# Optimization experiments

Hardware: AMD Instinct MI355X
Metric: run time of the kernel (lower is better)

The kernel has to match this reference:

```python
import jax, jax.numpy as jnp
import numpy as np

H, W = 200, 200           # BEV spatial shape (single level)
NBQ, NH, NL, NP = 2, 8, 1, 4
D = 256
HD = D // NH


def setup_inputs() -> dict:
    key = jax.random.key(0)
    ks = jax.random.split(key, 12)
    bs, nq = 1, H * W
    query = jax.random.normal(ks[0], (bs, nq, D), jnp.float32)
    value = jax.random.normal(ks[1], (bs, NBQ * nq, D), jnp.float32)
    reference_points = jax.random.uniform(ks[2], (bs, nq, NL, 2), dtype=jnp.float32)
    spatial_shapes = jnp.array([[H, W]], dtype=jnp.int32)
    sc = 1.0 / np.sqrt(D)
    W_v = jax.random.normal(ks[3], (D, D), jnp.float32) * sc
    b_v = jax.random.normal(ks[4], (D,), jnp.float32) * 0.01
    W_so = jax.random.normal(ks[5], (2 * D, NBQ * NH * NL * NP * 2), jnp.float32) * 0.02
    b_so = jax.random.normal(ks[6], (NBQ * NH * NL * NP * 2,), jnp.float32) * 0.5
    W_aw = jax.random.normal(ks[7], (2 * D, NBQ * NH * NL * NP), jnp.float32) * 0.02
    b_aw = jax.random.normal(ks[8], (NBQ * NH * NL * NP,), jnp.float32) * 0.01
    W_o = jax.random.normal(ks[9], (D, D), jnp.float32) * sc
    b_o = jax.random.normal(ks[10], (D,), jnp.float32) * 0.01
    return {"query": query, "value": value, "reference_points": reference_points,
            "spatial_shapes": spatial_shapes,
            "W_v": W_v, "b_v": b_v, "W_so": W_so, "b_so": b_so,
            "W_aw": W_aw, "b_aw": b_aw, "W_o": W_o, "b_o": b_o}


def _ms_deform_attn(value, locs, attn):
    # value: (B, K, NH, HD); locs: (B, nq, NH, NL, NP, 2) in [0,1]; attn: (B, nq, NH, NL, NP)
    B, K, h, d = value.shape
    nq = locs.shape[1]
    out = jnp.zeros((B, nq, h, d), value.dtype)
    start = 0
    for l, (Hl, Wl) in enumerate([(H, W)]):
        v = value[:, start:start + Hl * Wl].transpose(0, 2, 1, 3).reshape(B * h, Hl * Wl, d)
        start += Hl * Wl
        g = locs[:, :, :, l]                      # (B, nq, h, NP, 2)
        # grid_sample(align_corners=False, padding='zeros') pixel coords
        x = g[..., 0] * Wl - 0.5
        y = g[..., 1] * Hl - 0.5
        x0 = jnp.floor(x); y0 = jnp.floor(y)
        lx = x - x0; ly = y - y0
        x0 = x0.astype(jnp.int32); y0 = y0.astype(jnp.int32)
        acc = jnp.zeros((B * h, nq * NP, d), value.dtype)
        for dy, wy in ((0, 1.0 - ly), (1, ly)):
            for dx, wx in ((0, 1.0 - lx), (1, lx)):
                xi = x0 + dx; yi = y0 + dy
                valid = ((xi >= 0) & (xi < Wl) & (yi >= 0) & (yi < Hl)).astype(value.dtype)
                idx = jnp.clip(yi, 0, Hl - 1) * Wl + jnp.clip(xi, 0, Wl - 1)  # (B,nq,h,NP)
                idxf = idx.transpose(0, 2, 1, 3).reshape(B * h, nq * NP)
                samp = jnp.take_along_axis(v, idxf[:, :, None], axis=1)       # (B*h, nq*NP, d)
                wgt = (wx * wy * valid).transpose(0, 2, 1, 3).reshape(B * h, nq * NP, 1)
                acc = acc + samp * wgt
        acc = acc.reshape(B, h, nq, NP, d)
        out = out + jnp.einsum('bhqpd,bqhp->bqhd', acc, attn[:, :, :, l])
    return out.reshape(B, nq, h * d)


def reference(query, value, reference_points, spatial_shapes,
              W_v, b_v, W_so, b_so, W_aw, b_aw, W_o, b_o):
    bs, nq, _ = query.shape
    identity = query
    val4 = value.reshape(bs, NBQ, nq, D)
    # query enhanced with most recent bev-queue features
    qe = jnp.concatenate([val4[:, 0], query], axis=-1)           # (bs, nq, 2D)
    vproj = (value @ W_v + b_v).reshape(bs * NBQ, nq, NH, HD)
    off = (qe @ W_so + b_so).reshape(bs, nq, NH, NBQ, NL, NP, 2)
    aw = (qe @ W_aw + b_aw).reshape(bs, nq, NH, NBQ, NL * NP)
    aw = jax.nn.softmax(aw, axis=-1).reshape(bs, nq, NH, NBQ, NL, NP)
    aw = aw.transpose(0, 3, 1, 2, 4, 5).reshape(bs * NBQ, nq, NH, NL, NP)
    # offset normalizer: [W, H] per level
    norm = jnp.stack([spatial_shapes[:, 1], spatial_shapes[:, 0]], -1).astype(query.dtype)  # (NL,2)
    locs = (reference_points[:, :, None, None, :, None, :]
            + off / norm[None, None, None, None, :, None, :])     # (bs,nq,NH,NBQ,NL,NP,2)
    locs = locs.transpose(0, 3, 1, 2, 4, 5, 6).reshape(bs * NBQ, nq, NH, NL, NP, 2)
    out = _ms_deform_attn(vproj, locs, aw)                        # (bs*NBQ, nq, D)
    out = out.reshape(bs, NBQ, nq, D).mean(axis=1)
    return out @ W_o + b_o + identity
```

## Files before the change

### kernel.cpp

```cpp
#include <hip/hip_runtime.h>
#include <math.h>

#define HW_   40000
#define NQ_   40000
#define IMGW  200
#define IMGH  200

typedef __bf16 bf16;
typedef __attribute__((ext_vector_type(4))) __bf16 bf16x4;
typedef __attribute__((ext_vector_type(8))) __bf16 bf16x8;
typedef __attribute__((ext_vector_type(4))) float f32x4;

__device__ __forceinline__ void gload_lds16(const void* g, void* l) {
  __builtin_amdgcn_global_load_lds(
      (const __attribute__((address_space(1))) void*)g,
      (__attribute__((address_space(3))) void*)l, 16, 0, 0);
}

__global__ __launch_bounds__(256) void prep_kernel(
    const float* __restrict__ Wv, const float* __restrict__ Wso,
    const float* __restrict__ Waw, const float* __restrict__ Wo,
    bf16* __restrict__ BtV, bf16* __restrict__ BtOA, bf16* __restrict__ BtO)
{
  int idx = blockIdx.x * 256 + threadIdx.x;
  if (idx < 65536) {
    int k = idx >> 8, n = idx & 255;
    BtV[(size_t)n * 256 + k] = (bf16)Wv[idx];
  } else if (idx < 131072) {
    int j = idx - 65536;
    int k = j >> 7, n = j & 127;
    BtOA[(size_t)n * 512 + k] = (bf16)Wso[j];
  } else if (idx < 163840) {
    int j = idx - 131072;
    int k = j >> 6, n = j & 63;
    BtOA[(size_t)(128 + n) * 512 + k] = (bf16)Waw[j];
  } else if (idx < 229376) {
    int j = idx - 163840;
    int k = j >> 8, n = j & 255;
    BtO[(size_t)n * 256 + k] = (bf16)Wo[j];
  }
}

template<int KT, int MODE, int BN, int ASRC>
__global__ __launch_bounds__(256) void mfma_gemm_kernel(
    const void* __restrict__ A0, const void* __restrict__ A1,
    const bf16* __restrict__ Bt,
    const float* __restrict__ bias0, const float* __restrict__ bias1,
    const float* __restrict__ resid,
    void* __restrict__ outp, void* __restrict__ outp2, int M)
{
  constexpr int NT16 = BN / 32;
  constexpr int NCH  = BN * 4;
  constexpr int BCHN = (NCH + 255) / 256;
  constexpr int NIT  = KT / 32;
  __shared__ bf16 As[2][64 * 32];
  __shared__ bf16 Bs[2][BN * 32];
  const int t    = threadIdx.x;
  const int m0   = blockIdx.x * 64;
  const int n0   = blockIdx.y * BN;
  const int w    = t >> 6;
  const int lane = t & 63;
  const int quad = lane >> 4;
  const int l16  = lane & 15;
  const int wm   = (w & 1) * 32;
  const int wn   = (w >> 1) * (BN / 2);

  f32x4 acc[2][NT16] = {};

  int gmA;
  {
    int gm = m0 + (t >> 2);
    gmA = (gm >= M) ? (M - 1) : gm;
  }
  const int arow = t >> 2;
  const int akey = (arow >> 1) & 3;

  float4 apf[2];
  bf16x8 ah0, ah1;

  auto issueB = [&](int it) {
    const int kt  = it * 32;
    const int buf = it & 1;
#pragma unroll
    for (int i = 0; i < BCHN; ++i) {
      int c = i * 256 + t;
      if (NCH % 256 != 0 && c >= NCH) break;
      int row = c >> 2;
      int j   = (c & 3) ^ ((row >> 1) & 3);
      gload_lds16(&Bt[(size_t)(n0 + row) * KT + kt + j * 8], &Bs[buf][c * 8]);
    }
  };

  auto loadA_reg = [&](int it) {
    const int kt = it * 32;
    if (ASRC == 1) {
      const float* Ap; int col;
      if (KT == 512) { Ap = (kt < 256) ? (const float*)A0 : (const float*)A1; col = kt & 255; }
      else           { Ap = (const float*)A0; col = kt; }
      const float4* s4 = (const float4*)&Ap[(size_t)gmA * 256 + col + (t & 3) * 8];
      apf[0] = s4[0];
      apf[1] = s4[1];
    } else {
      ah0 = *(const bf16x8*)&((const bf16*)A0)[(size_t)gmA * 256 + kt + (t & 3) * 8];
      ah1 = *(const bf16x8*)&((const bf16*)A1)[(size_t)gmA * 256 + kt + (t & 3) * 8];
    }
  };

  auto writeA = [&](int it) {
    const int buf = it & 1;
    int j = (t & 3) ^ akey;
    bf16x8 o;
    if (ASRC == 1) {
      o = bf16x8{(bf16)apf[0].x, (bf16)apf[0].y, (bf16)apf[0].z, (bf16)apf[0].w,
                 (bf16)apf[1].x, (bf16)apf[1].y, (bf16)apf[1].z, (bf16)apf[1].w};
    } else {
#pragma unroll
      for (int e = 0; e < 8; ++e)
        o[e] = (bf16)(0.5f * ((float)ah0[e] + (float)ah1[e]));
    }
    *(bf16x8*)&As[buf][arow * 32 + j * 8] = o;
  };

  loadA_reg(0); issueB(0); writeA(0);

#pragma unroll
  for (int it = 0; it < NIT; ++it) {
    __syncthreads();
    if (it + 1 < NIT) {
      issueB(it + 1);
      loadA_reg(it + 1);
    }
    const bf16* as = As[it & 1];
    const bf16* bs = Bs[it & 1];
    bf16x8 af[2], bfr[NT16];
#pragma unroll
    for (int x = 0; x < 2; ++x) {
      int row = wm + x * 16 + l16;
      af[x] = *(const bf16x8*)&as[row * 32 + (quad ^ ((row >> 1) & 3)) * 8];
    }
#pragma unroll
    for (int x = 0; x < NT16; ++x) {
      int row = wn + x * 16 + l16;
      bfr[x] = *(const bf16x8*)&bs[row * 32 + (quad ^ ((row >> 1) & 3)) * 8];
    }
#pragma unroll
    for (int mt = 0; mt < 2; ++mt)
#pragma unroll
      for (int nt = 0; nt < NT16; ++nt)
        acc[mt][nt] = __builtin_amdgcn_mfma_f32_16x16x32_bf16(
            af[mt], bfr[nt], acc[mt][nt], 0, 0, 0);
    if (it + 1 < NIT) writeA(it + 1);
  }

#pragma unroll
  for (int mt = 0; mt < 2; ++mt) {
#pragma unroll
    for (int r = 0; r < 4; ++r) {
      const int gm = m0 + wm + mt * 16 + quad * 4 + r;
      if (gm >= M) continue;
#pragma unroll
      for (int nt = 0; nt < NT16; ++nt) {
        const int gn = n0 + wn + nt * 16 + l16;
        float v = acc[mt][nt][r];
        if (MODE == 0) {
          int nbq = (gm >= HW_) ? 1 : 0;
          int pix = gm - nbq * HW_;
          int h = gn >> 5, hd = gn & 31;
          ((bf16*)outp)[(((size_t)(nbq * 8 + h) * HW_ + pix) << 5) + hd] =
              (bf16)(v + bias0[gn]);
        } else if (MODE == 1) {
          if (gn < 128) {
            int gg = gn >> 3, e = gn & 7;
            ((bf16*)outp)[((size_t)gg * NQ_ + gm) * 8 + e] = (bf16)(v + bias0[gn]);
          } else {
            int j = gn - 128;
            int gg = j >> 2, e = j & 3;
            ((bf16*)outp2)[((size_t)gg * NQ_ + gm) * 4 + e] = (bf16)(v + bias1[j]);
          }
        } else {
          ((float*)outp)[(size_t)gm * 256 + gn] =
              v + bias0[gn] + resid[(size_t)gm * 256 + gn];
        }
      }
    }
  }
}

__global__ __launch_bounds__(256) void deform_attn_kernel(
    const bf16* __restrict__ vws,
    const bf16* __restrict__ off_g,
    const bf16* __restrict__ aw_g,
    const float* __restrict__ ref,
    bf16* __restrict__ ms0,
    bf16* __restrict__ ms1)
{
  const int t    = threadIdx.x;
  const int w    = t >> 6;
  const int lane = t & 63;
  const int b    = blockIdx.x;
  const int nbq  = b / 5000;
  const int bb   = b - nbq * 5000;
  const int h    = bb & 7;
  const int qc   = bb >> 3;
  const int qi   = lane >> 2;
  const int sub  = lane & 3;
  const int q    = qc * 64 + w * 16 + qi;
  const int g    = h * 2 + nbq;
  bf16* msN = nbq ? ms1 : ms0;

  const float rx = ref[2 * q + 0] * (float)IMGW - 0.5f;
  const float ry = ref[2 * q + 1] * (float)IMGH - 0.5f;

  bf16x4 a4 = *(const bf16x4*)&aw_g[((size_t)g * NQ_ + q) * 4];
  float aa0 = (float)a4[0], aa1 = (float)a4[1], aa2 = (float)a4[2], aa3 = (float)a4[3];
  float mx = fmaxf(fmaxf(aa0, aa1), fmaxf(aa2, aa3));
  float e0 = __expf(aa0 - mx), e1 = __expf(aa1 - mx);
  float e2 = __expf(aa2 - mx), e3 = __expf(aa3 - mx);
  float inv = 1.0f / (e0 + e1 + e2 + e3);
  float w4[4] = {e0 * inv, e1 * inv, e2 * inv, e3 * inv};

  bf16x8 o8 = *(const bf16x8*)&off_g[((size_t)g * NQ_ + q) * 8];

  const bf16* vbase = vws + (((size_t)(nbq * 8 + h) * HW_) << 5) + sub * 8;

  float  ww[16];
  bf16x8 v[16];
#pragma unroll
  for (int p = 0; p < 4; ++p) {
    float x = rx + (float)o8[2 * p];
    float y = ry + (float)o8[2 * p + 1];
    float xf = floorf(x), yf = floorf(y);
    int   x0 = (int)xf,   y0 = (int)yf;
    float lx = x - xf,    ly = y - yf;
    int   x1 = x0 + 1,    y1 = y0 + 1;
    float w00 = (1.0f - lx) * (1.0f - ly);
    float w01 = lx * (1.0f - ly);
    float w10 = (1.0f - lx) * ly;
    float w11 = lx * ly;
    if (x0 < 0 || x0 >= IMGW) { w00 = 0.0f; w10 = 0.0f; }
    if (x1 < 0 || x1 >= IMGW) { w01 = 0.0f; w11 = 0.0f; }
    if (y0 < 0 || y0 >= IMGH) { w00 = 0.0f; w01 = 0.0f; }
    if (y1 < 0 || y1 >= IMGH) { w10 = 0.0f; w11 = 0.0f; }
    int xc0 = min(max(x0, 0), IMGW - 1), xc1 = min(max(x1, 0), IMGW - 1);
    int yc0 = min(max(y0, 0), IMGH - 1), yc1 = min(max(y1, 0), IMGH - 1);
    float wp = w4[p];
    ww[4 * p + 0] = wp * w00;
    ww[4 * p + 1] = wp * w01;
    ww[4 * p + 2] = wp * w10;
    ww[4 * p + 3] = wp * w11;
    v[4 * p + 0] = *(const bf16x8*)&vbase[(size_t)(yc0 * IMGW + xc0) << 5];
    v[4 * p + 1] = *(const bf16x8*)&vbase[(size_t)(yc0 * IMGW + xc1) << 5];
    v[4 * p + 2] = *(const bf16x8*)&vbase[(size_t)(yc1 * IMGW + xc0) << 5];
    v[4 * p + 3] = *(const bf16x8*)&vbase[(size_t)(yc1 * IMGW + xc1) << 5];
  }

  float acc[8] = {};
#pragma unroll
  for (int s = 0; s < 16; ++s)
#pragma unroll
    for (int j = 0; j < 8; ++j)
      acc[j] = fmaf(ww[s], (float)v[s][j], acc[j]);

  bf16x8 o;
#pragma unroll
  for (int j = 0; j < 8; ++j) o[j] = (bf16)acc[j];
  *(bf16x8*)&msN[(size_t)q * 256 + h * 32 + sub * 8] = o;
}

extern "C" void kernel_launch(void* const* d_in, const int* in_sizes, int n_in,
                              void* d_out, int out_size, void* d_ws, size_t ws_size,
                              hipStream_t stream) {
  const float* query = (const float*)d_in[0];
  const float* value = (const float*)d_in[1];
  const float* ref   = (const float*)d_in[2];
  const float* Wv  = (const float*)d_in[4];
  const float* bv  = (const float*)d_in[5];
  const float* Wso = (const float*)d_in[6];
  const float* bso = (const float*)d_in[7];
  const float* Waw = (const float*)d_in[8];
  const float* baw = (const float*)d_in[9];
  const float* Wo  = (const float*)d_in[10];
  const float* bo  = (const float*)d_in[11];
  float* out = (float*)d_out;

  char* p = (char*)d_ws;
  bf16* vws    = (bf16*)p; p += (size_t)2 * 8 * HW_ * 32 * 2;
  bf16* off_g  = (bf16*)p; p += (size_t)16 * NQ_ * 8 * 2;
  bf16* aw_g   = (bf16*)p; p += (size_t)16 * NQ_ * 4 * 2;
  bf16* ms0    = (bf16*)p; p += (size_t)NQ_ * 256 * 2;
  bf16* ms1    = (bf16*)p; p += (size_t)NQ_ * 256 * 2;
  bf16* BtV    = (bf16*)p; p += (size_t)256 * 256 * 2;
  bf16* BtOA   = (bf16*)p; p += (size_t)192 * 512 * 2;
  bf16* BtO    = (bf16*)p; p += (size_t)256 * 256 * 2;

  prep_kernel<<<896, 256, 0, stream>>>(Wv, Wso, Waw, Wo, BtV, BtOA, BtO);

  mfma_gemm_kernel<256, 0, 128, 1><<<dim3(1250, 2), 256, 0, stream>>>(
      value, nullptr, BtV, bv, nullptr, nullptr, vws, nullptr, 2 * HW_);
  mfma_gemm_kernel<512, 1, 96, 1><<<dim3(625, 2), 256, 0, stream>>>(
      value, query, BtOA, bso, baw, nullptr, off_g, aw_g, NQ_);
  deform_attn_kernel<<<10000, 256, 0, stream>>>(vws, off_g, aw_g, ref, ms0, ms1);
  mfma_gemm_kernel<256, 2, 128, 2><<<dim3(625, 2), 256, 0, stream>>>(
      ms0, ms1, BtO, bo, nullptr, query, out, nullptr, NQ_);
}
```

Measured before the change: 300.5 us.

## Reuse bf16 value cast, average queues in-kernel, and DMA A tiles to LDS

The value projection GEMM now also writes a bf16 copy of the first queue's value rows, and the offset/attention GEMM reads that copy directly into LDS instead of reloading and converting fp32. The deform-attention kernel handles both BEV queues in one wave and combines them with a lane shuffle, writing a single averaged buffer. The output GEMM then loads bf16 A through global_load_lds instead of averaging two inputs in registers. Together these cut global traffic and per-element conversion work. In exchange, the value GEMM does extra stores, and the deform kernel uses a different lane-to-query mapping.

```diff
diff --git a/kernel.cpp b/kernel.cpp
--- a/kernel.cpp
+++ b/kernel.cpp
@@ -41,7 +41,7 @@
   }
 }
 
-template<int KT, int MODE, int BN, int ASRC>
+template<int KT, int MODE, int BN, int ASRC, int EMIT>
 __global__ __launch_bounds__(256) void mfma_gemm_kernel(
     const void* __restrict__ A0, const void* __restrict__ A1,
     const bf16* __restrict__ Bt,
@@ -76,7 +76,6 @@
   const int akey = (arow >> 1) & 3;
 
   float4 apf[2];
-  bf16x8 ah0, ah1;
 
   auto issueB = [&](int it) {
     const int kt  = it * 32;
@@ -91,44 +90,55 @@
     }
   };
 
+  auto issueA_lds = [&](int it, const bf16* Ap) {
+    const int kt  = it * 32;
+    int j = (t & 3) ^ akey;
+    gload_lds16(&Ap[(size_t)gmA * 256 + kt + j * 8], &As[it & 1][t * 8]);
+  };
+
   auto loadA_reg = [&](int it) {
     const int kt = it * 32;
-    if (ASRC == 1) {
-      const float* Ap; int col;
-      if (KT == 512) { Ap = (kt < 256) ? (const float*)A0 : (const float*)A1; col = kt & 255; }
-      else           { Ap = (const float*)A0; col = kt; }
-      const float4* s4 = (const float4*)&Ap[(size_t)gmA * 256 + col + (t & 3) * 8];
-      apf[0] = s4[0];
-      apf[1] = s4[1];
-    } else {
-      ah0 = *(const bf16x8*)&((const bf16*)A0)[(size_t)gmA * 256 + kt + (t & 3) * 8];
-      ah1 = *(const bf16x8*)&((const bf16*)A1)[(size_t)gmA * 256 + kt + (t & 3) * 8];
-    }
+    const float* Ap = (ASRC == 3) ? (const float*)A1 : (const float*)A0;
+    const int col = kt & 255;
+    const float4* s4 = (const float4*)&Ap[(size_t)gmA * 256 + col + (t & 3) * 8];
+    apf[0] = s4[0];
+    apf[1] = s4[1];
   };
 
   auto writeA = [&](int it) {
+    const int kt  = it * 32;
     const int buf = it & 1;
     int j = (t & 3) ^ akey;
-    bf16x8 o;
-    if (ASRC == 1) {
-      o = bf16x8{(bf16)apf[0].x, (bf16)apf[0].y, (bf16)apf[0].z, (bf16)apf[0].w,
-                 (bf16)apf[1].x, (bf16)apf[1].y, (bf16)apf[1].z, (bf16)apf[1].w};
-    } else {
-#pragma unroll
-      for (int e = 0; e < 8; ++e)
-        o[e] = (bf16)(0.5f * ((float)ah0[e] + (float)ah1[e]));
-    }
+    bf16x8 o = {(bf16)apf[0].x, (bf16)apf[0].y, (bf16)apf[0].z, (bf16)apf[0].w,
+                (bf16)apf[1].x, (bf16)apf[1].y, (bf16)apf[1].z, (bf16)apf[1].w};
     *(bf16x8*)&As[buf][arow * 32 + j * 8] = o;
-  };
-
-  loadA_reg(0); issueB(0); writeA(0);
+    if (EMIT) {
+      if (blockIdx.y == 0 && gmA < 40000)
+        *(bf16x8*)&((bf16*)outp2)[(size_t)gmA * 256 + kt + (t & 3) * 8] = o;
+    }
+  };
+
+  auto stageA_issue = [&](int it) {
+    if (ASRC == 0)      issueA_lds(it, (const bf16*)A0);
+    else if (ASRC == 1) loadA_reg(it);
+    else {
+      if (it * 32 < 256) issueA_lds(it, (const bf16*)A0);
+      else               loadA_reg(it);
+    }
+  };
+  auto stageA_write = [&](int it) {
+    if (ASRC == 1)                         writeA(it);
+    else if (ASRC == 3 && it * 32 >= 256)  writeA(it);
+  };
+
+  stageA_issue(0); issueB(0); stageA_write(0);
 
 #pragma unroll
   for (int it = 0; it < NIT; ++it) {
     __syncthreads();
     if (it + 1 < NIT) {
       issueB(it + 1);
-      loadA_reg(it + 1);
+      stageA_issue(it + 1);
     }
     const bf16* as = As[it & 1];
     const bf16* bs = Bs[it & 1];
@@ -149,7 +159,7 @@
       for (int nt = 0; nt < NT16; ++nt)
         acc[mt][nt] = __builtin_amdgcn_mfma_f32_16x16x32_bf16(
             af[mt], bfr[nt], acc[mt][nt], 0, 0, 0);
-    if (it + 1 < NIT) writeA(it + 1);
+    if (it + 1 < NIT) stageA_write(it + 1);
   }
 
 #pragma unroll
@@ -191,22 +201,18 @@
     const bf16* __restrict__ off_g,
     const bf16* __restrict__ aw_g,
     const float* __restrict__ ref,
-    bf16* __restrict__ ms0,
-    bf16* __restrict__ ms1)
+    bf16* __restrict__ ms)
 {
   const int t    = threadIdx.x;
   const int w    = t >> 6;
   const int lane = t & 63;
-  const int b    = blockIdx.x;
-  const int nbq  = b / 5000;
-  const int bb   = b - nbq * 5000;
-  const int h    = bb & 7;
-  const int qc   = bb >> 3;
-  const int qi   = lane >> 2;
+  const int h    = blockIdx.x & 7;
+  const int qb   = blockIdx.x >> 3;
+  const int qi   = lane >> 3;
+  const int nbq  = (lane >> 2) & 1;
   const int sub  = lane & 3;
-  const int q    = qc * 64 + w * 16 + qi;
+  const int q    = qb * 32 + w * 8 + qi;
   const int g    = h * 2 + nbq;
-  bf16* msN = nbq ? ms1 : ms0;
 
   const float rx = ref[2 * q + 0] * (float)IMGW - 0.5f;
   const float ry = ref[2 * q + 1] * (float)IMGH - 0.5f;
@@ -261,10 +267,15 @@
     for (int j = 0; j < 8; ++j)
       acc[j] = fmaf(ww[s], (float)v[s][j], acc[j]);
 
-  bf16x8 o;
-#pragma unroll
-  for (int j = 0; j < 8; ++j) o[j] = (bf16)acc[j];
-  *(bf16x8*)&msN[(size_t)q * 256 + h * 32 + sub * 8] = o;
+#pragma unroll
+  for (int j = 0; j < 8; ++j) acc[j] += __shfl_xor(acc[j], 4);
+
+  if (nbq == 0) {
+    bf16x8 o;
+#pragma unroll
+    for (int j = 0; j < 8; ++j) o[j] = (bf16)(0.5f * acc[j]);
+    *(bf16x8*)&ms[(size_t)q * 256 + h * 32 + sub * 8] = o;
+  }
 }
 
 extern "C" void kernel_launch(void* const* d_in, const int* in_sizes, int n_in,
@@ -287,19 +298,19 @@
   bf16* vws    = (bf16*)p; p += (size_t)2 * 8 * HW_ * 32 * 2;
   bf16* off_g  = (bf16*)p; p += (size_t)16 * NQ_ * 8 * 2;
   bf16* aw_g   = (bf16*)p; p += (size_t)16 * NQ_ * 4 * 2;
-  bf16* ms0    = (bf16*)p; p += (size_t)NQ_ * 256 * 2;
-  bf16* ms1    = (bf16*)p; p += (size_t)NQ_ * 256 * 2;
+  bf16* ms     = (bf16*)p; p += (size_t)NQ_ * 256 * 2;
+  bf16* val_bf = (bf16*)p; p += (size_t)NQ_ * 256 * 2;
   bf16* BtV    = (bf16*)p; p += (size_t)256 * 256 * 2;
   bf16* BtOA   = (bf16*)p; p += (size_t)192 * 512 * 2;
   bf16* BtO    = (bf16*)p; p += (size_t)256 * 256 * 2;
 
   prep_kernel<<<896, 256, 0, stream>>>(Wv, Wso, Waw, Wo, BtV, BtOA, BtO);
 
-  mfma_gemm_kernel<256, 0, 128, 1><<<dim3(1250, 2), 256, 0, stream>>>(
-      value, nullptr, BtV, bv, nullptr, nullptr, vws, nullptr, 2 * HW_);
-  mfma_gemm_kernel<512, 1, 96, 1><<<dim3(625, 2), 256, 0, stream>>>(
-      value, query, BtOA, bso, baw, nullptr, off_g, aw_g, NQ_);
-  deform_attn_kernel<<<10000, 256, 0, stream>>>(vws, off_g, aw_g, ref, ms0, ms1);
-  mfma_gemm_kernel<256, 2, 128, 2><<<dim3(625, 2), 256, 0, stream>>>(
-      ms0, ms1, BtO, bo, nullptr, query, out, nullptr, NQ_);
-}
+  mfma_gemm_kernel<256, 0, 128, 1, 1><<<dim3(1250, 2), 256, 0, stream>>>(
+      value, nullptr, BtV, bv, nullptr, nullptr, vws, val_bf, 2 * HW_);
+  mfma_gemm_kernel<512, 1, 96, 3, 0><<<dim3(625, 2), 256, 0, stream>>>(
+      val_bf, query, BtOA, bso, baw, nullptr, off_g, aw_g, NQ_);
+  deform_attn_kernel<<<10000, 256, 0, stream>>>(vws, off_g, aw_g, ref, ms);
+  mfma_gemm_kernel<256, 2, 128, 0, 0><<<dim3(625, 2), 256, 0, stream>>>(
+      ms, nullptr, BtO, bo, nullptr, query, out, nullptr, NQ_);
+}
```

Result: no change. 301.5 us (+0.3%).
